# Kernel optimization log

Hardware: AMD Instinct MI355X
Metric: run time of the kernel (lower is better)

## Reference

```python
import jax, jax.numpy as jnp
import numpy as np

N_NODES = 100000
N_GRAPHS = 512
HID = 128
IN_DIM = 128
OUT_DIM = 10
N_EDGES = 1600000


def gcn_conv(x, src, dst, W, b, n):
    # PyG GCNConv: add self-loops, symmetric normalization D^-1/2 (A+I) D^-1/2, then linear.
    h = x @ W  # [N, H]
    deg = jnp.zeros((n,), h.dtype).at[dst].add(1.0) + 1.0  # +1 self-loop
    dinv = jax.lax.rsqrt(deg)
    norm = dinv[src] * dinv[dst]  # [E]
    agg = jnp.zeros_like(h).at[dst].add(h[src] * norm[:, None])
    agg = agg + h * (dinv * dinv)[:, None]  # self-loop messages
    return agg + b


def setup_inputs() -> dict:
    key = jax.random.key(0)
    ks = jax.random.split(key, 12)
    x = jax.random.normal(ks[0], (N_NODES, IN_DIM), jnp.float32)
    edge_index = jax.random.randint(ks[1], (2, N_EDGES), 0, N_NODES)
    batch = jnp.sort(jax.random.randint(ks[2], (N_NODES,), 0, N_GRAPHS))
    def lin(k, fan_in, shape):
        bound = 1.0 / np.sqrt(fan_in)
        return jax.random.uniform(k, shape, jnp.float32, -bound, bound)
    W1 = lin(ks[3], IN_DIM, (IN_DIM, HID)); b1 = lin(ks[4], IN_DIM, (HID,))
    W2 = lin(ks[5], HID, (HID, HID)); b2 = lin(ks[6], HID, (HID,))
    W3 = lin(ks[7], HID, (HID, HID)); b3 = lin(ks[8], HID, (HID,))
    Wc1 = lin(ks[9], 2 * HID, (2 * HID, HID)); bc1 = lin(ks[9], 2 * HID, (HID,))
    Wc2 = lin(ks[10], HID, (HID, OUT_DIM)); bc2 = lin(ks[11], HID, (OUT_DIM,))
    return {"x": x, "edge_index": edge_index, "batch": batch,
            "W1": W1, "b1": b1, "W2": W2, "b2": b2, "W3": W3, "b3": b3,
            "Wc1": Wc1, "bc1": bc1, "Wc2": Wc2, "bc2": bc2}


def reference(x, edge_index, batch, W1, b1, W2, b2, W3, b3, Wc1, bc1, Wc2, bc2):
    src, dst = edge_index[0], edge_index[1]
    n = x.shape[0]
    h = jax.nn.relu(gcn_conv(x, src, dst, W1, b1, n))
    h = jax.nn.relu(gcn_conv(h, src, dst, W2, b2, n))
    h = gcn_conv(h, src, dst, W3, b3, n)  # no relu after last conv
    # global mean pool
    sums = jax.ops.segment_sum(h, batch, num_segments=N_GRAPHS)
    cnt = jax.ops.segment_sum(jnp.ones((n,), h.dtype), batch, num_segments=N_GRAPHS)
    mean = sums / jnp.maximum(cnt, 1.0)[:, None]
    # global max pool
    mx = jax.ops.segment_max(h, batch, num_segments=N_GRAPHS)
    mx = jnp.where(jnp.isfinite(mx), mx, 0.0)
    g = jnp.concatenate([mean, mx], axis=1)  # [G, 2H]
    g = jax.nn.relu(g @ Wc1 + bc1)
    return g @ Wc2 + bc2
```

## Files before the change

kernel.cpp:

```cpp
#include <hip/hip_runtime.h>

#define H 128
#define CAP 64
#define NB 128
#define BPCAP 2560
#define EPB 4096
#define SWLD 136

typedef __attribute__((ext_vector_type(8))) short bf16x8;
typedef __attribute__((ext_vector_type(4))) float f32x4;
typedef __attribute__((ext_vector_type(2))) float f32x2;

__device__ __forceinline__ unsigned short f2bf(float f) {
  unsigned u = __float_as_uint(f);
  unsigned r = u + 0x7FFFu + ((u >> 16) & 1u);
  return (unsigned short)(r >> 16);
}
__device__ __forceinline__ f32x2 up2(unsigned u) {
  return (f32x2){__uint_as_float(u << 16), __uint_as_float(u & 0xFFFF0000u)};
}

__global__ __launch_bounds__(256) void setup_all(
    const float* __restrict__ W1, const float* __restrict__ W2, const float* __restrict__ W3,
    unsigned short* __restrict__ Wt,
    const int* __restrict__ batch, int* __restrict__ g_start, int G,
    unsigned short* __restrict__ P, unsigned short* __restrict__ Q,
    int* __restrict__ bcount, int nbc, int n) {
  long long i = (long long)blockIdx.x * 256 + threadIdx.x;
  if (i < 3 * H * H) {
    int w = (int)(i >> 14);
    int rem = (int)i & (H * H - 1);
    int c = rem >> 7;
    int k = rem & 127;
    const float* W = (w == 0) ? W1 : (w == 1) ? W2 : W3;
    Wt[i] = f2bf(W[(size_t)k * H + c]);
    return;
  }
  i -= 3 * H * H;
  if (i < n) {
    int ii = (int)i;
    int b = batch[ii];
    int prev = (ii == 0) ? -1 : batch[ii - 1];
    for (int g = prev + 1; g <= b; ++g) g_start[g] = ii;
    if (ii == n - 1) {
      for (int g = b + 1; g <= G; ++g) g_start[g] = n;
    }
    return;
  }
  i -= n;
  if (i < H) {
    P[(size_t)n * H + i] = 0;
    Q[(size_t)n * H + i] = 0;
    return;
  }
  i -= H;
  if (i < nbc) bcount[i] = 0;
}

__global__ __launch_bounds__(512) void split1(
    const int* __restrict__ src, const int* __restrict__ dst,
    int2* __restrict__ buckets, int* __restrict__ bcount,
    int ne, int nbuck) {
  __shared__ int cnt[1024];
  __shared__ int gbase[1024];
  int tid = threadIdx.x;
  cnt[tid] = 0; cnt[tid + 512] = 0;
  __syncthreads();

  int beg = blockIdx.x * EPB;
  int end = beg + EPB; if (end > ne) end = ne;

  for (int e = beg + tid; e < end; e += 512) {
    int d = dst[e];
    atomicAdd(&cnt[d >> 7], 1);
  }
  __syncthreads();
  for (int i = tid; i < nbuck; i += 512) {
    int c = cnt[i];
    gbase[i] = (c > 0) ? atomicAdd(&bcount[i * 16], c) : 0;
    cnt[i] = 0;
  }
  __syncthreads();
  for (int e = beg + tid; e < end; e += 512) {
    int s = src[e];
    int d = dst[e];
    int b = d >> 7;
    int l = atomicAdd(&cnt[b], 1);
    int pos = gbase[b] + l;
    if (pos < BPCAP) buckets[(size_t)b * BPCAP + pos] = make_int2(s, d);
  }
}

__global__ __launch_bounds__(512) void build_csr(
    const int2* __restrict__ buckets, const int* __restrict__ bcount,
    int* __restrict__ csr_src, int* __restrict__ deg, float* __restrict__ dinv,
    int n) {
  __shared__ int rows[NB * CAP];
  __shared__ int cur[NB];
  int b = blockIdx.x;
  int tid = threadIdx.x;
  if (tid < NB) cur[tid] = 0;
  __syncthreads();
  int cntb = bcount[b * 16]; if (cntb > BPCAP) cntb = BPCAP;
  const int2* bp = buckets + (size_t)b * BPCAP;
  for (int i = tid; i < cntb; i += 512) {
    int2 e = bp[i];
    int r = e.y & (NB - 1);
    int slot = atomicAdd(&cur[r], 1);
    if (slot < CAP) rows[r * CAP + slot] = e.x;
  }
  __syncthreads();
  int4* gdst = (int4*)(csr_src + (size_t)b * NB * CAP);
  const int4* lsrc = (const int4*)rows;
#pragma unroll
  for (int i = tid; i < NB * CAP / 4; i += 512) gdst[i] = lsrc[i];
  if (tid < NB) {
    int node = b * NB + tid;
    if (node < n) {
      int d = cur[tid];
      deg[node] = d;
      dinv[node] = rsqrtf((float)(d + 1));
    }
  }
}

template <bool AF32>
__global__ __launch_bounds__(256) void gemm_mfma(
    const void* __restrict__ Av, const unsigned short* __restrict__ Wt,
    const float* __restrict__ dinv, unsigned short* __restrict__ outb, int n) {
  __shared__ unsigned short sW[H * SWLD];
  int tid = threadIdx.x;
  {
    int c = tid >> 1, hh = tid & 1;
    const int4* s = (const int4*)(Wt + (size_t)c * H + hh * 64);
    int4* d = (int4*)(sW + (size_t)c * SWLD + hh * 64);
#pragma unroll
    for (int i = 0; i < 8; ++i) d[i] = s[i];
  }
  __syncthreads();

  int wave = tid >> 6;
  int lane = tid & 63;
  int m = lane & 15;
  int quad = lane >> 4;
  int row = blockIdx.x * 64 + wave * 16 + m;
  bool rv = row < n;

  f32x4 acc[8];
#pragma unroll
  for (int t = 0; t < 8; ++t) acc[t] = (f32x4){0.f, 0.f, 0.f, 0.f};

#pragma unroll
  for (int k0 = 0; k0 < H; k0 += 32) {
    bf16x8 af;
    if (rv) {
      if (AF32) {
        const float* arow = (const float*)Av + (size_t)row * H + k0 + quad * 8;
        float4 f0 = *(const float4*)(arow + 0);
        float4 f1 = *(const float4*)(arow + 4);
        af[0] = (short)f2bf(f0.x); af[1] = (short)f2bf(f0.y);
        af[2] = (short)f2bf(f0.z); af[3] = (short)f2bf(f0.w);
        af[4] = (short)f2bf(f1.x); af[5] = (short)f2bf(f1.y);
        af[6] = (short)f2bf(f1.z); af[7] = (short)f2bf(f1.w);
      } else {
        const unsigned short* arow = (const unsigned short*)Av + (size_t)row * H;
        af = *(const bf16x8*)(arow + k0 + quad * 8);
      }
    } else {
      af = (bf16x8){0, 0, 0, 0, 0, 0, 0, 0};
    }
#pragma unroll
    for (int ct = 0; ct < 8; ++ct) {
      bf16x8 bfr = *(const bf16x8*)(sW + (size_t)(ct * 16 + m) * SWLD + k0 + quad * 8);
      acc[ct] = __builtin_amdgcn_mfma_f32_16x16x32_bf16(af, bfr, acc[ct], 0, 0, 0);
    }
  }

  __syncthreads();
  unsigned short (*sOut)[SWLD] = (unsigned short (*)[SWLD])sW;
  int r0 = wave * 16 + quad * 4;
#pragma unroll
  for (int r = 0; r < 4; ++r) {
    int orow = blockIdx.x * 64 + r0 + r;
    float dv = (orow < n) ? dinv[orow] : 0.f;
#pragma unroll
    for (int ct = 0; ct < 8; ++ct)
      sOut[r0 + r][ct * 16 + m] = f2bf(acc[ct][r] * dv);
  }
  __syncthreads();
  {
    int orow = blockIdx.x * 64 + (tid >> 2);
    if (orow < n) {
      const unsigned short* sp = &sOut[tid >> 2][(tid & 3) * 32];
      int4 t0 = *(const int4*)(sp + 0);
      int4 t1 = *(const int4*)(sp + 8);
      int4 t2 = *(const int4*)(sp + 16);
      int4 t3 = *(const int4*)(sp + 24);
      unsigned short* op = outb + (size_t)orow * H + (tid & 3) * 32;
      *(int4*)(op + 0)  = t0;
      *(int4*)(op + 8)  = t1;
      *(int4*)(op + 16) = t2;
      *(int4*)(op + 24) = t3;
    }
  }
}

template <bool RELU, bool OUTF32>
__global__ __launch_bounds__(256) void aggregate_bf(
    const unsigned short* __restrict__ hs, const int* __restrict__ deg_,
    const int* __restrict__ csr_src, const float* __restrict__ dinv,
    const float* __restrict__ b, void* __restrict__ outv, int n) {
  int node = blockIdx.x * 16 + (threadIdx.x >> 4);
  if (node >= n) return;
  int c = (threadIdx.x & 15) << 3;
  int deg = deg_[node]; if (deg > CAP) deg = CAP;
  int beg = node * CAP;
  int end = beg + ((deg + 7) & ~7);

  int4 sv = *(const int4*)(hs + (size_t)node * H + c);
  f32x2 a0 = up2(sv.x), a1 = up2(sv.y), a2 = up2(sv.z), a3 = up2(sv.w);

  int4 ia, ib;
  if (beg < end) {
    ia = *(const int4*)(csr_src + beg);
    ib = *(const int4*)(csr_src + beg + 4);
  }
  for (int k = beg; k < end; k += 8) {
    int4 ca = ia, cb = ib;
    int kn = k + 8;
    if (kn < end) {
      ia = *(const int4*)(csr_src + kn);
      ib = *(const int4*)(csr_src + kn + 4);
    }
    int rk = k - beg;
    if (rk + 8 > deg) {
      ca.x = (rk + 0 < deg) ? ca.x : n;
      ca.y = (rk + 1 < deg) ? ca.y : n;
      ca.z = (rk + 2 < deg) ? ca.z : n;
      ca.w = (rk + 3 < deg) ? ca.w : n;
      cb.x = (rk + 4 < deg) ? cb.x : n;
      cb.y = (rk + 5 < deg) ? cb.y : n;
      cb.z = (rk + 6 < deg) ? cb.z : n;
      cb.w = (rk + 7 < deg) ? cb.w : n;
    }
    int4 v0 = *(const int4*)(hs + (size_t)ca.x * H + c);
    int4 v1 = *(const int4*)(hs + (size_t)ca.y * H + c);
    int4 v2 = *(const int4*)(hs + (size_t)ca.z * H + c);
    int4 v3 = *(const int4*)(hs + (size_t)ca.w * H + c);
    int4 v4 = *(const int4*)(hs + (size_t)cb.x * H + c);
    int4 v5 = *(const int4*)(hs + (size_t)cb.y * H + c);
    int4 v6 = *(const int4*)(hs + (size_t)cb.z * H + c);
    int4 v7 = *(const int4*)(hs + (size_t)cb.w * H + c);
    a0 += ((up2(v0.x) + up2(v1.x)) + (up2(v2.x) + up2(v3.x))) +
          ((up2(v4.x) + up2(v5.x)) + (up2(v6.x) + up2(v7.x)));
    a1 += ((up2(v0.y) + up2(v1.y)) + (up2(v2.y) + up2(v3.y))) +
          ((up2(v4.y) + up2(v5.y)) + (up2(v6.y) + up2(v7.y)));
    a2 += ((up2(v0.z) + up2(v1.z)) + (up2(v2.z) + up2(v3.z))) +
          ((up2(v4.z) + up2(v5.z)) + (up2(v6.z) + up2(v7.z)));
    a3 += ((up2(v0.w) + up2(v1.w)) + (up2(v2.w) + up2(v3.w))) +
          ((up2(v4.w) + up2(v5.w)) + (up2(v6.w) + up2(v7.w)));
  }

  float dv = dinv[node];
  float4 b0 = *(const float4*)(b + c);
  float4 b1 = *(const float4*)(b + c + 4);
  float o0 = fmaf(a0.x, dv, b0.x), o1 = fmaf(a0.y, dv, b0.y);
  float o2 = fmaf(a1.x, dv, b0.z), o3 = fmaf(a1.y, dv, b0.w);
  float o4 = fmaf(a2.x, dv, b1.x), o5 = fmaf(a2.y, dv, b1.y);
  float o6 = fmaf(a3.x, dv, b1.z), o7 = fmaf(a3.y, dv, b1.w);
  if (RELU) {
    o0 = fmaxf(o0, 0.f); o1 = fmaxf(o1, 0.f); o2 = fmaxf(o2, 0.f); o3 = fmaxf(o3, 0.f);
    o4 = fmaxf(o4, 0.f); o5 = fmaxf(o5, 0.f); o6 = fmaxf(o6, 0.f); o7 = fmaxf(o7, 0.f);
  }
  if (OUTF32) {
    float* fo = (float*)outv + (size_t)node * H + c;
    *(float4*)(fo + 0) = make_float4(o0, o1, o2, o3);
    *(float4*)(fo + 4) = make_float4(o4, o5, o6, o7);
  } else {
    int4 ob;
    ob.x = ((unsigned)f2bf(o1) << 16) | f2bf(o0);
    ob.y = ((unsigned)f2bf(o3) << 16) | f2bf(o2);
    ob.z = ((unsigned)f2bf(o5) << 16) | f2bf(o4);
    ob.w = ((unsigned)f2bf(o7) << 16) | f2bf(o6);
    *(int4*)((unsigned short*)outv + (size_t)node * H + c) = ob;
  }
}

__global__ __launch_bounds__(256) void pool2(
    const float* __restrict__ h, const int* __restrict__ g_start,
    float* __restrict__ gmean, float* __restrict__ gmax, int n) {
  __shared__ float ssum[16][64];
  __shared__ float smax[16][64];
  int g = blockIdx.x >> 1;
  int half = blockIdx.x & 1;
  int beg = g_start[g];
  int end = g_start[g + 1];
  int q = threadIdx.x >> 4;
  int c = (threadIdx.x & 15) << 2;
  int cg = half * 64 + c;

  float4 s = make_float4(0.f, 0.f, 0.f, 0.f);
  float4 m = make_float4(-INFINITY, -INFINITY, -INFINITY, -INFINITY);
  for (int node = beg + q; node < end; node += 16) {
    float4 v = *(const float4*)(h + (size_t)node * H + cg);
    s.x += v.x; s.y += v.y; s.z += v.z; s.w += v.w;
    m.x = fmaxf(m.x, v.x); m.y = fmaxf(m.y, v.y);
    m.z = fmaxf(m.z, v.z); m.w = fmaxf(m.w, v.w);
  }
  *(float4*)&ssum[q][c] = s;
  *(float4*)&smax[q][c] = m;
  __syncthreads();

  int cnt = end - beg;
  int t = threadIdx.x;
  if (t < 64) {
    float tot = 0.f;
#pragma unroll
    for (int qq = 0; qq < 16; ++qq) tot += ssum[qq][t];
    gmean[(size_t)g * H + half * 64 + t] = tot / fmaxf((float)cnt, 1.0f);
  } else if (t < 128) {
    int cc = t - 64;
    float mx = -INFINITY;
#pragma unroll
    for (int qq = 0; qq < 16; ++qq) mx = fmaxf(mx, smax[qq][cc]);
    gmax[(size_t)g * H + half * 64 + cc] = (cnt == 0) ? 0.0f : mx;
  }
}

__global__ __launch_bounds__(128) void classify_kernel(
    const float* __restrict__ gmean, const float* __restrict__ gmax,
    const float* __restrict__ Wc1, const float* __restrict__ bc1,
    const float* __restrict__ Wc2, const float* __restrict__ bc2,
    float* __restrict__ out) {
  __shared__ float gv[2 * H];
  __shared__ float hid[H];
  int gid = blockIdx.x;
  int t = threadIdx.x;
  gv[t] = gmean[(size_t)gid * H + t];
  gv[H + t] = gmax[(size_t)gid * H + t];
  __syncthreads();
  float acc = 0.f;
#pragma unroll 8
  for (int k = 0; k < 2 * H; ++k) acc = fmaf(gv[k], Wc1[(size_t)k * H + t], acc);
  hid[t] = fmaxf(acc + bc1[t], 0.f);
  __syncthreads();
  if (t < 10) {
    float a2 = 0.f;
    for (int j = 0; j < H; ++j) a2 = fmaf(hid[j], Wc2[(size_t)j * 10 + t], a2);
    out[(size_t)gid * 10 + t] = a2 + bc2[t];
  }
}

extern "C" void kernel_launch(void* const* d_in, const int* in_sizes, int n_in,
                              void* d_out, int out_size, void* d_ws, size_t ws_size,
                              hipStream_t stream) {
  const float* x    = (const float*)d_in[0];
  const int* ei     = (const int*)d_in[1];
  const int* batch  = (const int*)d_in[2];
  const float* W1   = (const float*)d_in[3];
  const float* b1   = (const float*)d_in[4];
  const float* W2   = (const float*)d_in[5];
  const float* b2   = (const float*)d_in[6];
  const float* W3   = (const float*)d_in[7];
  const float* b3   = (const float*)d_in[8];
  const float* Wc1  = (const float*)d_in[9];
  const float* bc1  = (const float*)d_in[10];
  const float* Wc2  = (const float*)d_in[11];
  const float* bc2  = (const float*)d_in[12];
  float* out = (float*)d_out;

  const int n  = in_sizes[2];
  const int ne = in_sizes[1] / 2;
  const int G  = 512;
  const size_t NFb = (size_t)(n + 1) * H;

  const int* src = ei;
  const int* dst = ei + ne;

  const int nbuck = (n + NB - 1) / NB;
  const int nbc   = nbuck * 16;

  unsigned short* P_bf = (unsigned short*)d_ws;
  unsigned short* Q_bf = P_bf + NFb;
  float*          F2f  = (float*)(Q_bf + NFb);
  int* csr_src = (int*)(F2f + (size_t)n * H);
  const size_t csr_cap = (size_t)nbuck * NB * CAP;
  char* p = (char*)(csr_src + csr_cap);
  int*            deg      = (int*)p;            p += (size_t)n * 4;
  float*          dinv     = (float*)p;          p += (size_t)n * 4;
  int*            g_start  = (int*)p;            p += (size_t)(G + 1) * 4;
  float*          gmean    = (float*)p;          p += (size_t)G * H * 4;
  float*          gmax     = (float*)p;          p += (size_t)G * H * 4;
  p = (char*)(((uintptr_t)p + 255) & ~(uintptr_t)255);
  unsigned short* Wt       = (unsigned short*)p; p += (size_t)3 * H * H * 2;
  p = (char*)(((uintptr_t)p + 63) & ~(uintptr_t)63);
  int*            bcount   = (int*)p;            p += (size_t)nbc * 4;
  int2*           buckets  = (int2*)Q_bf;

  {
    long long tot = (long long)3 * H * H + n + H + nbc;
    int blocks = (int)((tot + 255) / 256);
    setup_all<<<blocks, 256, 0, stream>>>(W1, W2, W3, Wt, batch, g_start, G,
                                          P_bf, Q_bf, bcount, nbc, n);
  }

  split1<<<(ne + EPB - 1) / EPB, 512, 0, stream>>>(src, dst, buckets, bcount, ne, nbuck);
  build_csr<<<nbuck, 512, 0, stream>>>(buckets, bcount, csr_src, deg, dinv, n);

  const int tile_grid = (n + 63) / 64;
  const int node_grid = (n + 15) / 16;

  gemm_mfma<true><<<tile_grid, 256, 0, stream>>>(x, Wt, dinv, Q_bf, n);
  aggregate_bf<true, false><<<node_grid, 256, 0, stream>>>(Q_bf, deg, csr_src, dinv, b1, P_bf, n);

  gemm_mfma<false><<<tile_grid, 256, 0, stream>>>(P_bf, Wt + H * H, dinv, Q_bf, n);
  aggregate_bf<true, false><<<node_grid, 256, 0, stream>>>(Q_bf, deg, csr_src, dinv, b2, P_bf, n);

  gemm_mfma<false><<<tile_grid, 256, 0, stream>>>(P_bf, Wt + 2 * H * H, dinv, Q_bf, n);
  aggregate_bf<false, true><<<node_grid, 256, 0, stream>>>(Q_bf, deg, csr_src, dinv, b3, F2f, n);

  pool2<<<2 * G, 256, 0, stream>>>(F2f, g_start, gmean, gmax, n);
  classify_kernel<<<G, 128, 0, stream>>>(gmean, gmax, Wc1, bc1, Wc2, bc2, out);
}
```

Baseline: 440.9 us.

## Fuse all phases into one persistent cooperative kernel with grid syncs

Replaces the chain of ten separate kernel launches with one persistent cooperative kernel. Each phase runs as a grid-stride loop, and phases are separated by grid-wide barriers. Pooling and the classifier are also merged into a single per-graph phase. The aim is to remove launch gaps and tail effects between phases. In exchange, the shared buffer is sized for the largest phase, which limits occupancy, and every phase moves from 512 to 256 threads per block. The GEMM also reloads its weight tile for every tile it processes.

```diff
diff --git a/kernel.cpp b/kernel.cpp
--- a/kernel.cpp
+++ b/kernel.cpp
@@ -1,4 +1,7 @@
 #include <hip/hip_runtime.h>
+#include <hip/hip_cooperative_groups.h>
+
+namespace cg = cooperative_groups;
 
 #define H 128
 #define CAP 64
@@ -6,10 +9,22 @@
 #define BPCAP 2560
 #define EPB 4096
 #define SWLD 136
+#define SMEM_BYTES 35840
 
 typedef __attribute__((ext_vector_type(8))) short bf16x8;
 typedef __attribute__((ext_vector_type(4))) float f32x4;
 typedef __attribute__((ext_vector_type(2))) float f32x2;
+
+struct GArgs {
+  const float* x; const int* src; const int* dst; const int* batch;
+  const float *W1, *W2, *W3, *b1, *b2, *b3, *Wc1, *bc1, *Wc2, *bc2;
+  float* out;
+  unsigned short *P, *Q, *Wt;
+  float* F2f;
+  int* csr; int* deg; float* dinv; int* g_start; int* bcount;
+  int2* buckets;
+  int n, ne, nbuck, nbc, G;
+};
 
 __device__ __forceinline__ unsigned short f2bf(float f) {
   unsigned u = __float_as_uint(f);
@@ -20,405 +35,433 @@
   return (f32x2){__uint_as_float(u << 16), __uint_as_float(u & 0xFFFF0000u)};
 }
 
-__global__ __launch_bounds__(256) void setup_all(
-    const float* __restrict__ W1, const float* __restrict__ W2, const float* __restrict__ W3,
-    unsigned short* __restrict__ Wt,
-    const int* __restrict__ batch, int* __restrict__ g_start, int G,
-    unsigned short* __restrict__ P, unsigned short* __restrict__ Q,
-    int* __restrict__ bcount, int nbc, int n) {
-  long long i = (long long)blockIdx.x * 256 + threadIdx.x;
-  if (i < 3 * H * H) {
-    int w = (int)(i >> 14);
-    int rem = (int)i & (H * H - 1);
-    int c = rem >> 7;
-    int k = rem & 127;
-    const float* W = (w == 0) ? W1 : (w == 1) ? W2 : W3;
-    Wt[i] = f2bf(W[(size_t)k * H + c]);
-    return;
-  }
-  i -= 3 * H * H;
-  if (i < n) {
-    int ii = (int)i;
-    int b = batch[ii];
-    int prev = (ii == 0) ? -1 : batch[ii - 1];
-    for (int g = prev + 1; g <= b; ++g) g_start[g] = ii;
-    if (ii == n - 1) {
-      for (int g = b + 1; g <= G; ++g) g_start[g] = n;
-    }
-    return;
-  }
-  i -= n;
-  if (i < H) {
-    P[(size_t)n * H + i] = 0;
-    Q[(size_t)n * H + i] = 0;
-    return;
-  }
-  i -= H;
-  if (i < nbc) bcount[i] = 0;
-}
-
-__global__ __launch_bounds__(512) void split1(
-    const int* __restrict__ src, const int* __restrict__ dst,
-    int2* __restrict__ buckets, int* __restrict__ bcount,
-    int ne, int nbuck) {
-  __shared__ int cnt[1024];
-  __shared__ int gbase[1024];
+__device__ void ph_init_d(const GArgs& a) {
+  long long base = (long long)blockIdx.x * 256 + threadIdx.x;
+  long long stride = (long long)gridDim.x * 256;
+  long long tot = (long long)3 * H * H + a.n + H + a.nbc;
+  for (long long i0 = base; i0 < tot; i0 += stride) {
+    long long i = i0;
+    if (i < 3 * H * H) {
+      int w = (int)(i >> 14);
+      int rem = (int)i & (H * H - 1);
+      int c = rem >> 7;
+      int k = rem & 127;
+      const float* W = (w == 0) ? a.W1 : (w == 1) ? a.W2 : a.W3;
+      a.Wt[i] = f2bf(W[(size_t)k * H + c]);
+      continue;
+    }
+    i -= 3 * H * H;
+    if (i < a.n) {
+      int ii = (int)i;
+      int b = a.batch[ii];
+      int prev = (ii == 0) ? -1 : a.batch[ii - 1];
+      for (int g = prev + 1; g <= b; ++g) a.g_start[g] = ii;
+      if (ii == a.n - 1) {
+        for (int g = b + 1; g <= a.G; ++g) a.g_start[g] = a.n;
+      }
+      continue;
+    }
+    i -= a.n;
+    if (i < H) {
+      a.P[(size_t)a.n * H + i] = 0;
+      a.Q[(size_t)a.n * H + i] = 0;
+      continue;
+    }
+    i -= H;
+    a.bcount[i] = 0;
+  }
+}
+
+__device__ void ph_split_d(const GArgs& a, char* smem) {
+  int* cnt = (int*)smem;
+  int* gbase = cnt + 1024;
   int tid = threadIdx.x;
-  cnt[tid] = 0; cnt[tid + 512] = 0;
-  __syncthreads();
-
-  int beg = blockIdx.x * EPB;
-  int end = beg + EPB; if (end > ne) end = ne;
-
-  for (int e = beg + tid; e < end; e += 512) {
-    int d = dst[e];
-    atomicAdd(&cnt[d >> 7], 1);
-  }
-  __syncthreads();
-  for (int i = tid; i < nbuck; i += 512) {
-    int c = cnt[i];
-    gbase[i] = (c > 0) ? atomicAdd(&bcount[i * 16], c) : 0;
-    cnt[i] = 0;
-  }
-  __syncthreads();
-  for (int e = beg + tid; e < end; e += 512) {
-    int s = src[e];
-    int d = dst[e];
-    int b = d >> 7;
-    int l = atomicAdd(&cnt[b], 1);
-    int pos = gbase[b] + l;
-    if (pos < BPCAP) buckets[(size_t)b * BPCAP + pos] = make_int2(s, d);
-  }
-}
-
-__global__ __launch_bounds__(512) void build_csr(
-    const int2* __restrict__ buckets, const int* __restrict__ bcount,
-    int* __restrict__ csr_src, int* __restrict__ deg, float* __restrict__ dinv,
-    int n) {
-  __shared__ int rows[NB * CAP];
-  __shared__ int cur[NB];
-  int b = blockIdx.x;
+  int nchunk = (a.ne + EPB - 1) / EPB;
+  for (int ch = blockIdx.x; ch < nchunk; ch += gridDim.x) {
+    for (int i = tid; i < 1024; i += 256) cnt[i] = 0;
+    __syncthreads();
+    int beg = ch * EPB;
+    int end = beg + EPB; if (end > a.ne) end = a.ne;
+    for (int e = beg + tid; e < end; e += 256) atomicAdd(&cnt[a.dst[e] >> 7], 1);
+    __syncthreads();
+    for (int i = tid; i < a.nbuck; i += 256) {
+      int c = cnt[i];
+      gbase[i] = (c > 0) ? atomicAdd(&a.bcount[i * 16], c) : 0;
+      cnt[i] = 0;
+    }
+    __syncthreads();
+    for (int e = beg + tid; e < end; e += 256) {
+      int s = a.src[e];
+      int d = a.dst[e];
+      int b = d >> 7;
+      int l = atomicAdd(&cnt[b], 1);
+      int pos = gbase[b] + l;
+      if (pos < BPCAP) a.buckets[(size_t)b * BPCAP + pos] = make_int2(s, d);
+    }
+    __syncthreads();
+  }
+}
+
+__device__ void ph_build_d(const GArgs& a, char* smem) {
+  int* rows = (int*)smem;
+  int* cur = rows + NB * CAP;
   int tid = threadIdx.x;
-  if (tid < NB) cur[tid] = 0;
-  __syncthreads();
-  int cntb = bcount[b * 16]; if (cntb > BPCAP) cntb = BPCAP;
-  const int2* bp = buckets + (size_t)b * BPCAP;
-  for (int i = tid; i < cntb; i += 512) {
-    int2 e = bp[i];
-    int r = e.y & (NB - 1);
-    int slot = atomicAdd(&cur[r], 1);
-    if (slot < CAP) rows[r * CAP + slot] = e.x;
-  }
-  __syncthreads();
-  int4* gdst = (int4*)(csr_src + (size_t)b * NB * CAP);
-  const int4* lsrc = (const int4*)rows;
-#pragma unroll
-  for (int i = tid; i < NB * CAP / 4; i += 512) gdst[i] = lsrc[i];
-  if (tid < NB) {
-    int node = b * NB + tid;
-    if (node < n) {
-      int d = cur[tid];
-      deg[node] = d;
-      dinv[node] = rsqrtf((float)(d + 1));
-    }
-  }
-}
-
-template <bool AF32>
-__global__ __launch_bounds__(256) void gemm_mfma(
-    const void* __restrict__ Av, const unsigned short* __restrict__ Wt,
-    const float* __restrict__ dinv, unsigned short* __restrict__ outb, int n) {
-  __shared__ unsigned short sW[H * SWLD];
+  for (int b = blockIdx.x; b < a.nbuck; b += gridDim.x) {
+    if (tid < NB) cur[tid] = 0;
+    __syncthreads();
+    int cntb = a.bcount[b * 16]; if (cntb > BPCAP) cntb = BPCAP;
+    const int2* bp = a.buckets + (size_t)b * BPCAP;
+    for (int i = tid; i < cntb; i += 256) {
+      int2 e = bp[i];
+      int r = e.y & (NB - 1);
+      int slot = atomicAdd(&cur[r], 1);
+      if (slot < CAP) rows[r * CAP + slot] = e.x;
+    }
+    __syncthreads();
+    int4* gdst = (int4*)(a.csr + (size_t)b * NB * CAP);
+    const int4* lsrc = (const int4*)rows;
+    for (int i = tid; i < NB * CAP / 4; i += 256) gdst[i] = lsrc[i];
+    if (tid < NB) {
+      int node = b * NB + tid;
+      if (node < a.n) {
+        int d = cur[tid];
+        a.deg[node] = d;
+        a.dinv[node] = rsqrtf((float)(d + 1));
+      }
+    }
+    __syncthreads();
+  }
+}
+
+__device__ void ph_gemm_d(const GArgs& a, char* smem, bool af32,
+                          const void* Av, const unsigned short* Wt,
+                          unsigned short* outb) {
+  unsigned short* sW = (unsigned short*)smem;
   int tid = threadIdx.x;
-  {
-    int c = tid >> 1, hh = tid & 1;
-    const int4* s = (const int4*)(Wt + (size_t)c * H + hh * 64);
-    int4* d = (int4*)(sW + (size_t)c * SWLD + hh * 64);
-#pragma unroll
-    for (int i = 0; i < 8; ++i) d[i] = s[i];
-  }
-  __syncthreads();
-
   int wave = tid >> 6;
   int lane = tid & 63;
   int m = lane & 15;
   int quad = lane >> 4;
-  int row = blockIdx.x * 64 + wave * 16 + m;
-  bool rv = row < n;
-
-  f32x4 acc[8];
-#pragma unroll
-  for (int t = 0; t < 8; ++t) acc[t] = (f32x4){0.f, 0.f, 0.f, 0.f};
-
-#pragma unroll
-  for (int k0 = 0; k0 < H; k0 += 32) {
-    bf16x8 af;
-    if (rv) {
-      if (AF32) {
-        const float* arow = (const float*)Av + (size_t)row * H + k0 + quad * 8;
-        float4 f0 = *(const float4*)(arow + 0);
-        float4 f1 = *(const float4*)(arow + 4);
-        af[0] = (short)f2bf(f0.x); af[1] = (short)f2bf(f0.y);
-        af[2] = (short)f2bf(f0.z); af[3] = (short)f2bf(f0.w);
-        af[4] = (short)f2bf(f1.x); af[5] = (short)f2bf(f1.y);
-        af[6] = (short)f2bf(f1.z); af[7] = (short)f2bf(f1.w);
+  int ntile = (a.n + 63) / 64;
+  for (int t = blockIdx.x; t < ntile; t += gridDim.x) {
+    {
+      int cc = tid >> 1, hh = tid & 1;
+      const int4* s = (const int4*)(Wt + (size_t)cc * H + hh * 64);
+      int4* d = (int4*)(sW + (size_t)cc * SWLD + hh * 64);
+#pragma unroll
+      for (int i = 0; i < 8; ++i) d[i] = s[i];
+    }
+    __syncthreads();
+
+    int row = t * 64 + wave * 16 + m;
+    bool rv = row < a.n;
+    f32x4 acc[8];
+#pragma unroll
+    for (int q = 0; q < 8; ++q) acc[q] = (f32x4){0.f, 0.f, 0.f, 0.f};
+
+#pragma unroll
+    for (int k0 = 0; k0 < H; k0 += 32) {
+      bf16x8 af;
+      if (rv) {
+        if (af32) {
+          const float* arow = (const float*)Av + (size_t)row * H + k0 + quad * 8;
+          float4 f0 = *(const float4*)(arow + 0);
+          float4 f1 = *(const float4*)(arow + 4);
+          af[0] = (short)f2bf(f0.x); af[1] = (short)f2bf(f0.y);
+          af[2] = (short)f2bf(f0.z); af[3] = (short)f2bf(f0.w);
+          af[4] = (short)f2bf(f1.x); af[5] = (short)f2bf(f1.y);
+          af[6] = (short)f2bf(f1.z); af[7] = (short)f2bf(f1.w);
+        } else {
+          const unsigned short* arow = (const unsigned short*)Av + (size_t)row * H;
+          af = *(const bf16x8*)(arow + k0 + quad * 8);
+        }
       } else {
-        const unsigned short* arow = (const unsigned short*)Av + (size_t)row * H;
-        af = *(const bf16x8*)(arow + k0 + quad * 8);
-      }
+        af = (bf16x8){0, 0, 0, 0, 0, 0, 0, 0};
+      }
+#pragma unroll
+      for (int ct = 0; ct < 8; ++ct) {
+        bf16x8 bfr = *(const bf16x8*)(sW + (size_t)(ct * 16 + m) * SWLD + k0 + quad * 8);
+        acc[ct] = __builtin_amdgcn_mfma_f32_16x16x32_bf16(af, bfr, acc[ct], 0, 0, 0);
+      }
+    }
+
+    __syncthreads();
+    unsigned short (*sOut)[SWLD] = (unsigned short (*)[SWLD])sW;
+    int r0 = wave * 16 + quad * 4;
+#pragma unroll
+    for (int r = 0; r < 4; ++r) {
+      int orow = t * 64 + r0 + r;
+      float dv = (orow < a.n) ? a.dinv[orow] : 0.f;
+#pragma unroll
+      for (int ct = 0; ct < 8; ++ct)
+        sOut[r0 + r][ct * 16 + m] = f2bf(acc[ct][r] * dv);
+    }
+    __syncthreads();
+    {
+      int orow = t * 64 + (tid >> 2);
+      if (orow < a.n) {
+        const unsigned short* sp = &sOut[tid >> 2][(tid & 3) * 32];
+        int4 t0 = *(const int4*)(sp + 0);
+        int4 t1 = *(const int4*)(sp + 8);
+        int4 t2 = *(const int4*)(sp + 16);
+        int4 t3 = *(const int4*)(sp + 24);
+        unsigned short* op = outb + (size_t)orow * H + (tid & 3) * 32;
+        *(int4*)(op + 0)  = t0;
+        *(int4*)(op + 8)  = t1;
+        *(int4*)(op + 16) = t2;
+        *(int4*)(op + 24) = t3;
+      }
+    }
+    __syncthreads();
+  }
+}
+
+__device__ void ph_agg_d(const GArgs& a, const unsigned short* hs,
+                         const float* bias, void* outv, bool relu, bool outf32) {
+  int n = a.n;
+  int ngrp = (n + 15) / 16;
+  for (int g = blockIdx.x; g < ngrp; g += gridDim.x) {
+    int node = g * 16 + (threadIdx.x >> 4);
+    if (node >= n) continue;
+    int c = (threadIdx.x & 15) << 3;
+    int deg = a.deg[node]; if (deg > CAP) deg = CAP;
+    int beg = node * CAP;
+    int end = beg + ((deg + 7) & ~7);
+
+    int4 sv = *(const int4*)(hs + (size_t)node * H + c);
+    f32x2 a0 = up2(sv.x), a1 = up2(sv.y), a2 = up2(sv.z), a3 = up2(sv.w);
+
+    int4 ia, ib;
+    if (beg < end) {
+      ia = *(const int4*)(a.csr + beg);
+      ib = *(const int4*)(a.csr + beg + 4);
+    }
+    for (int k = beg; k < end; k += 8) {
+      int4 ca = ia, cb = ib;
+      int kn = k + 8;
+      if (kn < end) {
+        ia = *(const int4*)(a.csr + kn);
+        ib = *(const int4*)(a.csr + kn + 4);
+      }
+      int rk = k - beg;
+      if (rk + 8 > deg) {
+        ca.x = (rk + 0 < deg) ? ca.x : n;
+        ca.y = (rk + 1 < deg) ? ca.y : n;
+        ca.z = (rk + 2 < deg) ? ca.z : n;
+        ca.w = (rk + 3 < deg) ? ca.w : n;
+        cb.x = (rk + 4 < deg) ? cb.x : n;
+        cb.y = (rk + 5 < deg) ? cb.y : n;
+        cb.z = (rk + 6 < deg) ? cb.z : n;
+        cb.w = (rk + 7 < deg) ? cb.w : n;
+      }
+      int4 v0 = *(const int4*)(hs + (size_t)ca.x * H + c);
+      int4 v1 = *(const int4*)(hs + (size_t)ca.y * H + c);
+      int4 v2 = *(const int4*)(hs + (size_t)ca.z * H + c);
+      int4 v3 = *(const int4*)(hs + (size_t)ca.w * H + c);
+      int4 v4 = *(const int4*)(hs + (size_t)cb.x * H + c);
+      int4 v5 = *(const int4*)(hs + (size_t)cb.y * H + c);
+      int4 v6 = *(const int4*)(hs + (size_t)cb.z * H + c);
+      int4 v7 = *(const int4*)(hs + (size_t)cb.w * H + c);
+      a0 += ((up2(v0.x) + up2(v1.x)) + (up2(v2.x) + up2(v3.x))) +
+            ((up2(v4.x) + up2(v5.x)) + (up2(v6.x) + up2(v7.x)));
+      a1 += ((up2(v0.y) + up2(v1.y)) + (up2(v2.y) + up2(v3.y))) +
+            ((up2(v4.y) + up2(v5.y)) + (up2(v6.y) + up2(v7.y)));
+      a2 += ((up2(v0.z) + up2(v1.z)) + (up2(v2.z) + up2(v3.z))) +
+            ((up2(v4.z) + up2(v5.z)) + (up2(v6.z) + up2(v7.z)));
+      a3 += ((up2(v0.w) + up2(v1.w)) + (up2(v2.w) + up2(v3.w))) +
+            ((up2(v4.w) + up2(v5.w)) + (up2(v6.w) + up2(v7.w)));
+    }
+
+    float dv = a.dinv[node];
+    float4 b0 = *(const float4*)(bias + c);
+    float4 b1 = *(const float4*)(bias + c + 4);
+    float o0 = fmaf(a0.x, dv, b0.x), o1 = fmaf(a0.y, dv, b0.y);
+    float o2 = fmaf(a1.x, dv, b0.z), o3 = fmaf(a1.y, dv, b0.w);
+    float o4 = fmaf(a2.x, dv, b1.x), o5 = fmaf(a2.y, dv, b1.y);
+    float o6 = fmaf(a3.x, dv, b1.z), o7 = fmaf(a3.y, dv, b1.w);
+    if (relu) {
+      o0 = fmaxf(o0, 0.f); o1 = fmaxf(o1, 0.f); o2 = fmaxf(o2, 0.f); o3 = fmaxf(o3, 0.f);
+      o4 = fmaxf(o4, 0.f); o5 = fmaxf(o5, 0.f); o6 = fmaxf(o6, 0.f); o7 = fmaxf(o7, 0.f);
+    }
+    if (outf32) {
+      float* fo = (float*)outv + (size_t)node * H + c;
+      *(float4*)(fo + 0) = make_float4(o0, o1, o2, o3);
+      *(float4*)(fo + 4) = make_float4(o4, o5, o6, o7);
     } else {
-      af = (bf16x8){0, 0, 0, 0, 0, 0, 0, 0};
-    }
-#pragma unroll
-    for (int ct = 0; ct < 8; ++ct) {
-      bf16x8 bfr = *(const bf16x8*)(sW + (size_t)(ct * 16 + m) * SWLD + k0 + quad * 8);
-      acc[ct] = __builtin_amdgcn_mfma_f32_16x16x32_bf16(af, bfr, acc[ct], 0, 0, 0);
-    }
-  }
-
-  __syncthreads();
-  unsigned short (*sOut)[SWLD] = (unsigned short (*)[SWLD])sW;
-  int r0 = wave * 16 + quad * 4;
-#pragma unroll
-  for (int r = 0; r < 4; ++r) {
-    int orow = blockIdx.x * 64 + r0 + r;
-    float dv = (orow < n) ? dinv[orow] : 0.f;
-#pragma unroll
-    for (int ct = 0; ct < 8; ++ct)
-      sOut[r0 + r][ct * 16 + m] = f2bf(acc[ct][r] * dv);
-  }
-  __syncthreads();
-  {
-    int orow = blockIdx.x * 64 + (tid >> 2);
-    if (orow < n) {
-      const unsigned short* sp = &sOut[tid >> 2][(tid & 3) * 32];
-      int4 t0 = *(const int4*)(sp + 0);
-      int4 t1 = *(const int4*)(sp + 8);
-      int4 t2 = *(const int4*)(sp + 16);
-      int4 t3 = *(const int4*)(sp + 24);
-      unsigned short* op = outb + (size_t)orow * H + (tid & 3) * 32;
-      *(int4*)(op + 0)  = t0;
-      *(int4*)(op + 8)  = t1;
-      *(int4*)(op + 16) = t2;
-      *(int4*)(op + 24) = t3;
-    }
-  }
-}
-
-template <bool RELU, bool OUTF32>
-__global__ __launch_bounds__(256) void aggregate_bf(
-    const unsigned short* __restrict__ hs, const int* __restrict__ deg_,
-    const int* __restrict__ csr_src, const float* __restrict__ dinv,
-    const float* __restrict__ b, void* __restrict__ outv, int n) {
-  int node = blockIdx.x * 16 + (threadIdx.x >> 4);
-  if (node >= n) return;
-  int c = (threadIdx.x & 15) << 3;
-  int deg = deg_[node]; if (deg > CAP) deg = CAP;
-  int beg = node * CAP;
-  int end = beg + ((deg + 7) & ~7);
-
-  int4 sv = *(const int4*)(hs + (size_t)node * H + c);
-  f32x2 a0 = up2(sv.x), a1 = up2(sv.y), a2 = up2(sv.z), a3 = up2(sv.w);
-
-  int4 ia, ib;
-  if (beg < end) {
-    ia = *(const int4*)(csr_src + beg);
-    ib = *(const int4*)(csr_src + beg + 4);
-  }
-  for (int k = beg; k < end; k += 8) {
-    int4 ca = ia, cb = ib;
-    int kn = k + 8;
-    if (kn < end) {
-      ia = *(const int4*)(csr_src + kn);
-      ib = *(const int4*)(csr_src + kn + 4);
-    }
-    int rk = k - beg;
-    if (rk + 8 > deg) {
-      ca.x = (rk + 0 < deg) ? ca.x : n;
-      ca.y = (rk + 1 < deg) ? ca.y : n;
-      ca.z = (rk + 2 < deg) ? ca.z : n;
-      ca.w = (rk + 3 < deg) ? ca.w : n;
-      cb.x = (rk + 4 < deg) ? cb.x : n;
-      cb.y = (rk + 5 < deg) ? cb.y : n;
-      cb.z = (rk + 6 < deg) ? cb.z : n;
-      cb.w = (rk + 7 < deg) ? cb.w : n;
-    }
-    int4 v0 = *(const int4*)(hs + (size_t)ca.x * H + c);
-    int4 v1 = *(const int4*)(hs + (size_t)ca.y * H + c);
-    int4 v2 = *(const int4*)(hs + (size_t)ca.z * H + c);
-    int4 v3 = *(const int4*)(hs + (size_t)ca.w * H + c);
-    int4 v4 = *(const int4*)(hs + (size_t)cb.x * H + c);
-    int4 v5 = *(const int4*)(hs + (size_t)cb.y * H + c);
-    int4 v6 = *(const int4*)(hs + (size_t)cb.z * H + c);
-    int4 v7 = *(const int4*)(hs + (size_t)cb.w * H + c);
-    a0 += ((up2(v0.x) + up2(v1.x)) + (up2(v2.x) + up2(v3.x))) +
-          ((up2(v4.x) + up2(v5.x)) + (up2(v6.x) + up2(v7.x)));
-    a1 += ((up2(v0.y) + up2(v1.y)) + (up2(v2.y) + up2(v3.y))) +
-          ((up2(v4.y) + up2(v5.y)) + (up2(v6.y) + up2(v7.y)));
-    a2 += ((up2(v0.z) + up2(v1.z)) + (up2(v2.z) + up2(v3.z))) +
-          ((up2(v4.z) + up2(v5.z)) + (up2(v6.z) + up2(v7.z)));
-    a3 += ((up2(v0.w) + up2(v1.w)) + (up2(v2.w) + up2(v3.w))) +
-          ((up2(v4.w) + up2(v5.w)) + (up2(v6.w) + up2(v7.w)));
-  }
-
-  float dv = dinv[node];
-  float4 b0 = *(const float4*)(b + c);
-  float4 b1 = *(const float4*)(b + c + 4);
-  float o0 = fmaf(a0.x, dv, b0.x), o1 = fmaf(a0.y, dv, b0.y);
-  float o2 = fmaf(a1.x, dv, b0.z), o3 = fmaf(a1.y, dv, b0.w);
-  float o4 = fmaf(a2.x, dv, b1.x), o5 = fmaf(a2.y, dv, b1.y);
-  float o6 = fmaf(a3.x, dv, b1.z), o7 = fmaf(a3.y, dv, b1.w);
-  if (RELU) {
-    o0 = fmaxf(o0, 0.f); o1 = fmaxf(o1, 0.f); o2 = fmaxf(o2, 0.f); o3 = fmaxf(o3, 0.f);
-    o4 = fmaxf(o4, 0.f); o5 = fmaxf(o5, 0.f); o6 = fmaxf(o6, 0.f); o7 = fmaxf(o7, 0.f);
-  }
-  if (OUTF32) {
-    float* fo = (float*)outv + (size_t)node * H + c;
-    *(float4*)(fo + 0) = make_float4(o0, o1, o2, o3);
-    *(float4*)(fo + 4) = make_float4(o4, o5, o6, o7);
-  } else {
-    int4 ob;
-    ob.x = ((unsigned)f2bf(o1) << 16) | f2bf(o0);
-    ob.y = ((unsigned)f2bf(o3) << 16) | f2bf(o2);
-    ob.z = ((unsigned)f2bf(o5) << 16) | f2bf(o4);
-    ob.w = ((unsigned)f2bf(o7) << 16) | f2bf(o6);
-    *(int4*)((unsigned short*)outv + (size_t)node * H + c) = ob;
-  }
-}
-
-__global__ __launch_bounds__(256) void pool2(
-    const float* __restrict__ h, const int* __restrict__ g_start,
-    float* __restrict__ gmean, float* __restrict__ gmax, int n) {
-  __shared__ float ssum[16][64];
-  __shared__ float smax[16][64];
-  int g = blockIdx.x >> 1;
-  int half = blockIdx.x & 1;
-  int beg = g_start[g];
-  int end = g_start[g + 1];
-  int q = threadIdx.x >> 4;
-  int c = (threadIdx.x & 15) << 2;
-  int cg = half * 64 + c;
-
-  float4 s = make_float4(0.f, 0.f, 0.f, 0.f);
-  float4 m = make_float4(-INFINITY, -INFINITY, -INFINITY, -INFINITY);
-  for (int node = beg + q; node < end; node += 16) {
-    float4 v = *(const float4*)(h + (size_t)node * H + cg);
-    s.x += v.x; s.y += v.y; s.z += v.z; s.w += v.w;
-    m.x = fmaxf(m.x, v.x); m.y = fmaxf(m.y, v.y);
-    m.z = fmaxf(m.z, v.z); m.w = fmaxf(m.w, v.w);
-  }
-  *(float4*)&ssum[q][c] = s;
-  *(float4*)&smax[q][c] = m;
-  __syncthreads();
-
-  int cnt = end - beg;
+      int4 ob;
+      ob.x = ((unsigned)f2bf(o1) << 16) | f2bf(o0);
+      ob.y = ((unsigned)f2bf(o3) << 16) | f2bf(o2);
+      ob.z = ((unsigned)f2bf(o5) << 16) | f2bf(o4);
+      ob.w = ((unsigned)f2bf(o7) << 16) | f2bf(o6);
+      *(int4*)((unsigned short*)outv + (size_t)node * H + c) = ob;
+    }
+  }
+}
+
+__device__ void ph_poolcls_d(const GArgs& a, char* smem) {
+  float* ssum = (float*)smem;
+  float* smax = ssum + 8 * 128;
+  float* gv   = smax + 8 * 128;
+  float* hid  = gv + 256;
   int t = threadIdx.x;
-  if (t < 64) {
-    float tot = 0.f;
-#pragma unroll
-    for (int qq = 0; qq < 16; ++qq) tot += ssum[qq][t];
-    gmean[(size_t)g * H + half * 64 + t] = tot / fmaxf((float)cnt, 1.0f);
-  } else if (t < 128) {
-    int cc = t - 64;
-    float mx = -INFINITY;
-#pragma unroll
-    for (int qq = 0; qq < 16; ++qq) mx = fmaxf(mx, smax[qq][cc]);
-    gmax[(size_t)g * H + half * 64 + cc] = (cnt == 0) ? 0.0f : mx;
-  }
-}
-
-__global__ __launch_bounds__(128) void classify_kernel(
-    const float* __restrict__ gmean, const float* __restrict__ gmax,
-    const float* __restrict__ Wc1, const float* __restrict__ bc1,
-    const float* __restrict__ Wc2, const float* __restrict__ bc2,
-    float* __restrict__ out) {
-  __shared__ float gv[2 * H];
-  __shared__ float hid[H];
-  int gid = blockIdx.x;
-  int t = threadIdx.x;
-  gv[t] = gmean[(size_t)gid * H + t];
-  gv[H + t] = gmax[(size_t)gid * H + t];
-  __syncthreads();
-  float acc = 0.f;
+  for (int g = blockIdx.x; g < a.G; g += gridDim.x) {
+    int beg = a.g_start[g];
+    int end = a.g_start[g + 1];
+    int q = t >> 5;
+    int c = (t & 31) << 2;
+
+    float4 s = make_float4(0.f, 0.f, 0.f, 0.f);
+    float4 m = make_float4(-INFINITY, -INFINITY, -INFINITY, -INFINITY);
+    for (int node = beg + q; node < end; node += 8) {
+      float4 v = *(const float4*)(a.F2f + (size_t)node * H + c);
+      s.x += v.x; s.y += v.y; s.z += v.z; s.w += v.w;
+      m.x = fmaxf(m.x, v.x); m.y = fmaxf(m.y, v.y);
+      m.z = fmaxf(m.z, v.z); m.w = fmaxf(m.w, v.w);
+    }
+    *(float4*)&ssum[q * 128 + c] = s;
+    *(float4*)&smax[q * 128 + c] = m;
+    __syncthreads();
+
+    int cnt = end - beg;
+    if (t < 128) {
+      float tot = 0.f;
+#pragma unroll
+      for (int qq = 0; qq < 8; ++qq) tot += ssum[qq * 128 + t];
+      gv[t] = tot / fmaxf((float)cnt, 1.0f);
+    } else {
+      int cc = t - 128;
+      float mx = -INFINITY;
+#pragma unroll
+      for (int qq = 0; qq < 8; ++qq) mx = fmaxf(mx, smax[qq * 128 + cc]);
+      gv[H + cc] = (cnt == 0) ? 0.0f : mx;
+    }
+    __syncthreads();
+    if (t < H) {
+      float acc = 0.f;
 #pragma unroll 8
-  for (int k = 0; k < 2 * H; ++k) acc = fmaf(gv[k], Wc1[(size_t)k * H + t], acc);
-  hid[t] = fmaxf(acc + bc1[t], 0.f);
-  __syncthreads();
-  if (t < 10) {
-    float a2 = 0.f;
-    for (int j = 0; j < H; ++j) a2 = fmaf(hid[j], Wc2[(size_t)j * 10 + t], a2);
-    out[(size_t)gid * 10 + t] = a2 + bc2[t];
-  }
+      for (int k = 0; k < 2 * H; ++k) acc = fmaf(gv[k], a.Wc1[(size_t)k * H + t], acc);
+      hid[t] = fmaxf(acc + a.bc1[t], 0.f);
+    }
+    __syncthreads();
+    if (t < 10) {
+      float a2 = 0.f;
+      for (int j = 0; j < H; ++j) a2 = fmaf(hid[j], a.Wc2[(size_t)j * 10 + t], a2);
+      a.out[(size_t)g * 10 + t] = a2 + a.bc2[t];
+    }
+    __syncthreads();
+  }
+}
+
+__global__ __launch_bounds__(256, 4) void mega(GArgs a) {
+  __shared__ __align__(16) char smem[SMEM_BYTES];
+  cg::grid_group gg = cg::this_grid();
+  ph_init_d(a);
+  __threadfence(); gg.sync();
+  ph_split_d(a, smem);
+  __threadfence(); gg.sync();
+  ph_build_d(a, smem);
+  __threadfence(); gg.sync();
+  ph_gemm_d(a, smem, true, a.x, a.Wt, a.Q);
+  __threadfence(); gg.sync();
+  ph_agg_d(a, a.Q, a.b1, a.P, true, false);
+  __threadfence(); gg.sync();
+  ph_gemm_d(a, smem, false, a.P, a.Wt + H * H, a.Q);
+  __threadfence(); gg.sync();
+  ph_agg_d(a, a.Q, a.b2, a.P, true, false);
+  __threadfence(); gg.sync();
+  ph_gemm_d(a, smem, false, a.P, a.Wt + 2 * H * H, a.Q);
+  __threadfence(); gg.sync();
+  ph_agg_d(a, a.Q, a.b3, a.F2f, false, true);
+  __threadfence(); gg.sync();
+  ph_poolcls_d(a, smem);
+}
+
+__global__ __launch_bounds__(256) void k_init(GArgs a) { ph_init_d(a); }
+__global__ __launch_bounds__(256) void k_split(GArgs a) {
+  __shared__ __align__(16) char smem[8192];
+  ph_split_d(a, smem);
+}
+__global__ __launch_bounds__(256) void k_build(GArgs a) {
+  __shared__ __align__(16) char smem[NB * CAP * 4 + NB * 4];
+  ph_build_d(a, smem);
+}
+__global__ __launch_bounds__(256) void k_gemm(GArgs a, int L) {
+  __shared__ __align__(16) char smem[H * SWLD * 2];
+  if (L == 0)      ph_gemm_d(a, smem, true,  a.x, a.Wt,           a.Q);
+  else if (L == 1) ph_gemm_d(a, smem, false, a.P, a.Wt + H * H,   a.Q);
+  else             ph_gemm_d(a, smem, false, a.P, a.Wt + 2 * H * H, a.Q);
+}
+__global__ __launch_bounds__(256) void k_agg(GArgs a, int L) {
+  if (L == 0)      ph_agg_d(a, a.Q, a.b1, a.P,   true,  false);
+  else if (L == 1) ph_agg_d(a, a.Q, a.b2, a.P,   true,  false);
+  else             ph_agg_d(a, a.Q, a.b3, a.F2f, false, true);
+}
+__global__ __launch_bounds__(256) void k_poolcls(GArgs a) {
+  __shared__ __align__(16) char smem[10240];
+  ph_poolcls_d(a, smem);
 }
 
 extern "C" void kernel_launch(void* const* d_in, const int* in_sizes, int n_in,
                               void* d_out, int out_size, void* d_ws, size_t ws_size,
                               hipStream_t stream) {
-  const float* x    = (const float*)d_in[0];
-  const int* ei     = (const int*)d_in[1];
-  const int* batch  = (const int*)d_in[2];
-  const float* W1   = (const float*)d_in[3];
-  const float* b1   = (const float*)d_in[4];
-  const float* W2   = (const float*)d_in[5];
-  const float* b2   = (const float*)d_in[6];
-  const float* W3   = (const float*)d_in[7];
-  const float* b3   = (const float*)d_in[8];
-  const float* Wc1  = (const float*)d_in[9];
-  const float* bc1  = (const float*)d_in[10];
-  const float* Wc2  = (const float*)d_in[11];
-  const float* bc2  = (const float*)d_in[12];
-  float* out = (float*)d_out;
-
-  const int n  = in_sizes[2];
-  const int ne = in_sizes[1] / 2;
-  const int G  = 512;
-  const size_t NFb = (size_t)(n + 1) * H;
-
-  const int* src = ei;
-  const int* dst = ei + ne;
-
-  const int nbuck = (n + NB - 1) / NB;
-  const int nbc   = nbuck * 16;
-
-  unsigned short* P_bf = (unsigned short*)d_ws;
-  unsigned short* Q_bf = P_bf + NFb;
-  float*          F2f  = (float*)(Q_bf + NFb);
-  int* csr_src = (int*)(F2f + (size_t)n * H);
-  const size_t csr_cap = (size_t)nbuck * NB * CAP;
-  char* p = (char*)(csr_src + csr_cap);
-  int*            deg      = (int*)p;            p += (size_t)n * 4;
-  float*          dinv     = (float*)p;          p += (size_t)n * 4;
-  int*            g_start  = (int*)p;            p += (size_t)(G + 1) * 4;
-  float*          gmean    = (float*)p;          p += (size_t)G * H * 4;
-  float*          gmax     = (float*)p;          p += (size_t)G * H * 4;
+  GArgs a;
+  a.x    = (const float*)d_in[0];
+  const int* ei = (const int*)d_in[1];
+  a.batch = (const int*)d_in[2];
+  a.W1 = (const float*)d_in[3];  a.b1 = (const float*)d_in[4];
+  a.W2 = (const float*)d_in[5];  a.b2 = (const float*)d_in[6];
+  a.W3 = (const float*)d_in[7];  a.b3 = (const float*)d_in[8];
+  a.Wc1 = (const float*)d_in[9]; a.bc1 = (const float*)d_in[10];
+  a.Wc2 = (const float*)d_in[11]; a.bc2 = (const float*)d_in[12];
+  a.out = (float*)d_out;
+
+  a.n  = in_sizes[2];
+  a.ne = in_sizes[1] / 2;
+  a.G  = 512;
+  a.src = ei;
+  a.dst = ei + a.ne;
+  a.nbuck = (a.n + NB - 1) / NB;
+  a.nbc   = a.nbuck * 16;
+
+  const size_t NFb = (size_t)(a.n + 1) * H;
+
+  a.P   = (unsigned short*)d_ws;
+  a.Q   = a.P + NFb;
+  a.F2f = (float*)(a.Q + NFb);
+  a.csr = (int*)(a.F2f + (size_t)a.n * H);
+  const size_t csr_cap = (size_t)a.nbuck * NB * CAP;
+  char* p = (char*)(a.csr + csr_cap);
+  a.deg     = (int*)p;     p += (size_t)a.n * 4;
+  a.dinv    = (float*)p;   p += (size_t)a.n * 4;
+  a.g_start = (int*)p;     p += (size_t)(a.G + 1) * 4;
   p = (char*)(((uintptr_t)p + 255) & ~(uintptr_t)255);
-  unsigned short* Wt       = (unsigned short*)p; p += (size_t)3 * H * H * 2;
+  a.Wt      = (unsigned short*)p; p += (size_t)3 * H * H * 2;
   p = (char*)(((uintptr_t)p + 63) & ~(uintptr_t)63);
-  int*            bcount   = (int*)p;            p += (size_t)nbc * 4;
-  int2*           buckets  = (int2*)Q_bf;
-
-  {
-    long long tot = (long long)3 * H * H + n + H + nbc;
-    int blocks = (int)((tot + 255) / 256);
-    setup_all<<<blocks, 256, 0, stream>>>(W1, W2, W3, Wt, batch, g_start, G,
-                                          P_bf, Q_bf, bcount, nbc, n);
-  }
-
-  split1<<<(ne + EPB - 1) / EPB, 512, 0, stream>>>(src, dst, buckets, bcount, ne, nbuck);
-  build_csr<<<nbuck, 512, 0, stream>>>(buckets, bcount, csr_src, deg, dinv, n);
-
-  const int tile_grid = (n + 63) / 64;
-  const int node_grid = (n + 15) / 16;
-
-  gemm_mfma<true><<<tile_grid, 256, 0, stream>>>(x, Wt, dinv, Q_bf, n);
-  aggregate_bf<true, false><<<node_grid, 256, 0, stream>>>(Q_bf, deg, csr_src, dinv, b1, P_bf, n);
-
-  gemm_mfma<false><<<tile_grid, 256, 0, stream>>>(P_bf, Wt + H * H, dinv, Q_bf, n);
-  aggregate_bf<true, false><<<node_grid, 256, 0, stream>>>(Q_bf, deg, csr_src, dinv, b2, P_bf, n);
-
-  gemm_mfma<false><<<tile_grid, 256, 0, stream>>>(P_bf, Wt + 2 * H * H, dinv, Q_bf, n);
-  aggregate_bf<false, true><<<node_grid, 256, 0, stream>>>(Q_bf, deg, csr_src, dinv, b3, F2f, n);
-
-  pool2<<<2 * G, 256, 0, stream>>>(F2f, g_start, gmean, gmax, n);
-  classify_kernel<<<G, 128, 0, stream>>>(gmean, gmax, Wc1, bc1, Wc2, bc2, out);
-}
+  a.bcount  = (int*)p;     p += (size_t)a.nbc * 4;
+  a.buckets = (int2*)a.Q;
+
+  int maxb = 0;
+  hipError_t oe = hipOccupancyMaxActiveBlocksPerMultiprocessor(&maxb, mega, 256, 0);
+  hipError_t le = hipErrorUnknown;
+  if (oe == hipSuccess && maxb >= 1) {
+    int grid = maxb * 256;
+    if (grid > 2048) grid = 2048;
+    GArgs aa = a;
+    void* kargs[] = {&aa};
+    le = hipLaunchCooperativeKernel(reinterpret_cast<void*>(&mega),
+                                    dim3(grid), dim3(256), kargs, 0, stream);
+  }
+  if (le != hipSuccess) {
+    long long tot = (long long)3 * H * H + a.n + H + a.nbc;
+    k_init<<<(int)((tot + 255) / 256), 256, 0, stream>>>(a);
+    k_split<<<(a.ne + EPB - 1) / EPB, 256, 0, stream>>>(a);
+    k_build<<<a.nbuck, 256, 0, stream>>>(a);
+    const int tile_grid = (a.n + 63) / 64;
+    const int node_grid = (a.n + 15) / 16;
+    for (int L = 0; L < 3; ++L) {
+      k_gemm<<<tile_grid, 256, 0, stream>>>(a, L);
+      k_agg<<<node_grid, 256, 0, stream>>>(a, L);
+    }
+    k_poolcls<<<a.G, 256, 0, stream>>>(a);
+  }
+}
```

Result: slower. 1.550 ms (+251.5%).
